# Kernel tuning notes

Hardware: AMD Instinct MI355X
Metric: run time of the kernel (lower is better)

The kernel has to match this reference:

```python
import jax, jax.numpy as jnp
import numpy as np

E, H = 512, 8
D = E // H  # head_dim = 64
NEG = jnp.finfo(jnp.float32).min


def setup_inputs() -> dict:
    key = jax.random.key(0)
    ks = jax.random.split(key, 12)
    s = 0.02
    return {
        "image": jax.random.normal(ks[0], (16, 197, E), jnp.float32),
        "text": jax.random.normal(ks[1], (64, 30, E), jnp.float32),
        "text_mask": jax.random.randint(ks[2], (64, 29), 0, 2).astype(bool),
        "Wq": jax.random.normal(ks[3], (D, D), jnp.float32) * s,
        "Wk": jax.random.normal(ks[4], (D, D), jnp.float32) * s,
        "Wv": jax.random.normal(ks[5], (D, D), jnp.float32) * s,
        "W_out": jax.random.normal(ks[6], (E, E), jnp.float32) * s,
        "b_out": jnp.zeros((E,), jnp.float32),
        "Wtv": jax.random.normal(ks[7], (D, D), jnp.float32) * s,
        "W_out_text": jax.random.normal(ks[8], (E, E), jnp.float32) * s,
        "b_out_text": jnp.zeros((E,), jnp.float32),
    }


def reference(image, text, text_mask, Wq, Wk, Wv, W_out, b_out, Wtv, W_out_text, b_out_text):
    I, Q, _ = image.shape
    T, K, _ = text.shape
    img = image.reshape(I, Q, H, D)
    txt = text.reshape(T, K, H, D)
    # per-head linear projections (torch Linear: y = x @ W.T)
    q = img @ Wq.T            # [I,Q,H,D]
    k = txt @ Wk.T            # [T,K,H,D]
    v = txt @ Wv.T            # [T,K,H,D]
    # cross-batch bidirectional attention energy [I,T,H,Q,K]
    energy = jnp.einsum('tkhd,iqhd->ithqk', k, q)
    # cls_present: pad mask with True at front along K
    mask = jnp.pad(text_mask, ((0, 0), (1, 0)), constant_values=True)  # [T,K]
    energy = jnp.where(mask[None, :, None, None, :], energy, NEG)
    scaled = energy / jnp.sqrt(jnp.float32(E))
    attention = jax.nn.softmax(scaled, axis=-1)       # over k (i2t)
    text_attention = jax.nn.softmax(scaled, axis=-2)  # over q (t2i)
    # i2t branch: [I,T,Q,H,D] -> [I,T,Q,E]
    out = jnp.einsum('ithqk,tkhd->itqhd', attention, v).reshape(I, T, Q, E)
    out = out @ W_out.T + b_out
    out = out.mean(axis=2)  # mean pool over image tokens -> [I,T,E]
    # t2i branch: [I,T,K,H,D] -> [I,T,K,E]
    tv = img @ Wtv.T  # [I,Q,H,D]
    out_text = jnp.einsum('ithqk,iqhd->itkhd', text_attention, tv).reshape(I, T, K, E)
    out_text = out_text @ W_out_text.T + b_out_text
    out_text = out_text.mean(axis=2)  # mean pool over text tokens -> [I,T,E]
    return (out, out_text, attention, text_attention)
```

## Files before the change

### kernel.cpp

```cpp
#include <hip/hip_runtime.h>
#include <hip/hip_bf16.h>
#include <cstdint>

#define I_ 16
#define T_ 64
#define Q_ 197
#define K_ 30
#define H_ 8
#define D_ 64
#define E_ 512

typedef float f32x2 __attribute__((ext_vector_type(2)));
typedef float f32x4 __attribute__((ext_vector_type(4)));
typedef short bf16x8 __attribute__((ext_vector_type(8)));

static constexpr float INV_SQRT_E = 0.044194173824159216f;
static constexpr float C197 = 1.0f / 197.0f;

#define OFF_QBF   0
#define OFF_KBF   806912
#define OFF_V     1298432
#define OFF_TV    2281472
#define OFF_ASUM  3895296
#define OFF_TASUM 4141056
#define OFF_POUT  5754880
#define OFF_PTXT  6279168

__global__ __launch_bounds__(512) void proj_kernel(
    const float* __restrict__ image, const float* __restrict__ text,
    const float* __restrict__ Wq, const float* __restrict__ Wk,
    const float* __restrict__ Wv, const float* __restrict__ Wtv,
    float* __restrict__ ws)
{
  const int NQ4 = (I_ * Q_) / 4;
  const int NT4 = (T_ * K_) / 4;
  int bb = blockIdx.x;
  const float* X; const float* W; int row0; int mode;
  if (bb < NQ4)             { X = image; W = Wq;  row0 = bb * 4;               mode = 0; }
  else if (bb < NQ4 + NT4)  { X = text;  W = Wk;  row0 = (bb - NQ4) * 4;       mode = 1; }
  else if (bb < NQ4 + 2*NT4){ X = text;  W = Wv;  row0 = (bb - NQ4 - NT4) * 4; mode = 2; }
  else                      { X = image; W = Wtv; row0 = (bb - NQ4 - 2*NT4)*4; mode = 3; }

  __shared__ float s_x[4][E_];
  __shared__ float s_w[D_][D_ + 1];
  int tid = threadIdx.x;
  for (int idx = tid; idx < D_ * D_; idx += 512) s_w[idx >> 6][idx & 63] = W[idx];
  #pragma unroll
  for (int rr = 0; rr < 4; ++rr) s_x[rr][tid] = X[(size_t)(row0 + rr) * E_ + tid];
  __syncthreads();

  int h = tid >> 6, dout = tid & 63;
  float a0 = 0.f, a1 = 0.f, a2 = 0.f, a3 = 0.f;
  #pragma unroll
  for (int d = 0; d < D_; ++d) {
    float w = s_w[dout][d];
    a0 = fmaf(s_x[0][h * 64 + d], w, a0);
    a1 = fmaf(s_x[1][h * 64 + d], w, a1);
    a2 = fmaf(s_x[2][h * 64 + d], w, a2);
    a3 = fmaf(s_x[3][h * 64 + d], w, a3);
  }
  if (mode <= 1) {
    __hip_bfloat16* Y = (__hip_bfloat16*)(ws + (mode == 0 ? OFF_QBF : OFF_KBF));
    Y[(size_t)(row0 + 0) * E_ + tid] = __float2bfloat16(a0);
    Y[(size_t)(row0 + 1) * E_ + tid] = __float2bfloat16(a1);
    Y[(size_t)(row0 + 2) * E_ + tid] = __float2bfloat16(a2);
    Y[(size_t)(row0 + 3) * E_ + tid] = __float2bfloat16(a3);
  } else {
    float* Y = ws + (mode == 2 ? OFF_V : OFF_TV);
    Y[(size_t)(row0 + 0) * E_ + tid] = a0;
    Y[(size_t)(row0 + 1) * E_ + tid] = a1;
    Y[(size_t)(row0 + 2) * E_ + tid] = a2;
    Y[(size_t)(row0 + 3) * E_ + tid] = a3;
  }
}

__global__ __launch_bounds__(256, 8) void attn_kernel(
    const __hip_bfloat16* __restrict__ qbf, const __hip_bfloat16* __restrict__ kbf,
    const int* __restrict__ text_mask,
    float* __restrict__ attn_out, float* __restrict__ tattn_out,
    float* __restrict__ A_sum, float* __restrict__ TA_sum)
{
  int b = blockIdx.x;
  int h = b & 7, t = (b >> 3) & 63, i = b >> 9;
  int tid = threadIdx.x;
  int w = tid >> 6, lane = tid & 63;
  int lr = lane & 15, lg = lane >> 4;

  __shared__ __hip_bfloat16 s_e[208 * 30];
  __shared__ float s_invrow[208];
  __shared__ float s_cd[4][32];
  __shared__ float s_ca[4][32];
  __shared__ float s_invd[32];
  __shared__ int   s_mask[32];

  if (tid < 32) s_mask[tid] = (tid == 0) ? 1 : (tid < K_ ? text_mask[t * (K_ - 1) + tid - 1] : 0);

  int m0 = (lr == 0) ? 1 : text_mask[t * (K_ - 1) + lr - 1];
  int m1 = (lr < 14) ? text_mask[t * (K_ - 1) + 15 + lr] : 0;

  const __hip_bfloat16* qb = qbf + ((size_t)(i * Q_) * H_ + h) * D_;
  const __hip_bfloat16* kb = kbf + ((size_t)(t * K_) * H_ + h) * D_;

  const bf16x8* bp0 = (const bf16x8*)(kb + (size_t)lr * (H_ * D_) + lg * 8);
  const bf16x8* bp1 = (const bf16x8*)(kb + (size_t)(16 + lr) * (H_ * D_) + lg * 8);
  bf16x8 b00 = bp0[0], b01 = bp0[4];
  bf16x8 b10 = bp1[0], b11 = bp1[4];

  float cd0 = 0.f, cd1 = 0.f, ca0 = 0.f, ca1 = 0.f;

  #pragma unroll
  for (int j = 0; j < 4; ++j) {
    int mt = w + 4 * j;
    if (mt < 13) {
      const bf16x8* ap = (const bf16x8*)(qb + (size_t)(mt * 16 + lr) * (H_ * D_) + lg * 8);
      bf16x8 a0 = ap[0], a1 = ap[4];
      f32x4 acc0 = {0.f, 0.f, 0.f, 0.f}, acc1 = {0.f, 0.f, 0.f, 0.f};
      acc0 = __builtin_amdgcn_mfma_f32_16x16x32_bf16(a0, b00, acc0, 0, 0, 0);
      acc0 = __builtin_amdgcn_mfma_f32_16x16x32_bf16(a1, b01, acc0, 0, 0, 0);
      acc1 = __builtin_amdgcn_mfma_f32_16x16x32_bf16(a0, b10, acc1, 0, 0, 0);
      acc1 = __builtin_amdgcn_mfma_f32_16x16x32_bf16(a1, b11, acc1, 0, 0, 0);
      int row0 = mt * 16 + lg * 4;
      float v0[4], v1[4];
      #pragma unroll
      for (int r = 0; r < 4; ++r) {
        bool vr = (row0 + r) < Q_;
        v0[r] = (vr && m0) ? __expf(acc0[r] * INV_SQRT_E) : 0.f;
        v1[r] = (vr && m1) ? __expf(acc1[r] * INV_SQRT_E) : 0.f;
        s_e[(row0 + r) * K_ + lr] = __float2bfloat16(v0[r]);
        if (lr < 14) s_e[(row0 + r) * K_ + 16 + lr] = __float2bfloat16(v1[r]);
      }
      #pragma unroll
      for (int r = 0; r < 4; ++r) {
        float s = v0[r] + v1[r];
        s += __shfl_xor(s, 1);
        s += __shfl_xor(s, 2);
        s += __shfl_xor(s, 4);
        s += __shfl_xor(s, 8);
        float iv = ((row0 + r) < Q_ && s > 0.f) ? (1.0f / s) : 0.f;
        if (lr == 0) s_invrow[row0 + r] = iv;
        cd0 += v0[r]; ca0 += v0[r] * iv;
        cd1 += v1[r]; ca1 += v1[r] * iv;
      }
    }
  }

  cd0 += __shfl_xor(cd0, 16); cd0 += __shfl_xor(cd0, 32);
  ca0 += __shfl_xor(ca0, 16); ca0 += __shfl_xor(ca0, 32);
  cd1 += __shfl_xor(cd1, 16); cd1 += __shfl_xor(cd1, 32);
  ca1 += __shfl_xor(ca1, 16); ca1 += __shfl_xor(ca1, 32);
  if (lane < 16) {
    s_cd[w][lr] = cd0; s_cd[w][lr + 16] = cd1;
    s_ca[w][lr] = ca0; s_ca[w][lr + 16] = ca1;
  }
  __syncthreads();

  if (tid < 32) {
    int col = tid;
    float d  = s_cd[0][col] + s_cd[1][col] + s_cd[2][col] + s_cd[3][col];
    float pa = s_ca[0][col] + s_ca[1][col] + s_ca[2][col] + s_ca[3][col];
    s_invd[col] = (s_mask[col] && d > 0.f) ? (1.0f / d) : 0.f;
    if (col < K_) A_sum[(size_t)b * K_ + col] = pa;
  }
  __syncthreads();

  if (tid < Q_) {
    float ta = 0.f;
    #pragma unroll
    for (int kk = 0; kk < K_; ++kk) {
      float ev = __bfloat162float(s_e[tid * K_ + kk]);
      ta += s_mask[kk] ? ev * s_invd[kk] : C197;
    }
    TA_sum[(size_t)b * Q_ + tid] = ta;
  }

  {
    int r0 = tid >> 4;
    int c2 = tid & 15;
    if (c2 < 15) {
      int mc0 = s_mask[2 * c2], mc1 = s_mask[2 * c2 + 1];
      float inv0 = s_invd[2 * c2], inv1 = s_invd[2 * c2 + 1];
      f32x2* adst = (f32x2*)(attn_out + (size_t)b * (Q_ * K_));
      f32x2* tdst = (f32x2*)(tattn_out + (size_t)b * (Q_ * K_));
      for (int row = r0; row < Q_; row += 16) {
        __hip_bfloat162 ev2 = *(const __hip_bfloat162*)&s_e[row * K_ + 2 * c2];
        float ex = __bfloat162float(ev2.x);
        float ey = __bfloat162float(ev2.y);
        float ir = s_invrow[row];
        f32x2 av  = { ex * ir, ey * ir };
        f32x2 tv2 = { mc0 ? ex * inv0 : C197, mc1 ? ey * inv1 : C197 };
        int o = row * 15 + c2;
        __builtin_nontemporal_store(av, &adst[o]);
        __builtin_nontemporal_store(tv2, &tdst[o]);
      }
    }
  }
}

__global__ __launch_bounds__(512) void pool_fused_kernel(
    const float* __restrict__ A_sum, const float* __restrict__ TA_sum,
    const float* __restrict__ ws_v, const float* __restrict__ ws_tv,
    float* __restrict__ P_out, float* __restrict__ P_txt)
{
  int bt = blockIdx.x;
  int t = bt & 63;
  int i = bt >> 6;
  int tid = threadIdx.x;
  int h = tid >> 6, d = tid & 63;
  __shared__ float s_A[H_ * K_];
  __shared__ float s_TA[H_ * Q_];
  if (tid < H_ * K_) s_A[tid] = A_sum[(size_t)bt * H_ * K_ + tid];
  for (int idx = tid; idx < H_ * Q_; idx += 512) s_TA[idx] = TA_sum[(size_t)bt * H_ * Q_ + idx];
  __syncthreads();

  {
    float a0 = 0.f, a1 = 0.f;
    #pragma unroll
    for (int kk = 0; kk < K_; kk += 2) {
      a0 = fmaf(s_A[h * K_ + kk],     ws_v[((size_t)(t * K_ + kk)     * H_ + h) * D_ + d], a0);
      a1 = fmaf(s_A[h * K_ + kk + 1], ws_v[((size_t)(t * K_ + kk + 1) * H_ + h) * D_ + d], a1);
    }
    P_out[(size_t)bt * E_ + tid] = (a0 + a1) * (1.0f / 197.0f);
  }

  {
    float a0 = 0.f, a1 = 0.f, a2 = 0.f, a3 = 0.f;
    int qq = 0;
    for (; qq + 4 <= Q_; qq += 4) {
      a0 = fmaf(s_TA[h * Q_ + qq + 0], ws_tv[((size_t)(i * Q_ + qq + 0) * H_ + h) * D_ + d], a0);
      a1 = fmaf(s_TA[h * Q_ + qq + 1], ws_tv[((size_t)(i * Q_ + qq + 1) * H_ + h) * D_ + d], a1);
      a2 = fmaf(s_TA[h * Q_ + qq + 2], ws_tv[((size_t)(i * Q_ + qq + 2) * H_ + h) * D_ + d], a2);
      a3 = fmaf(s_TA[h * Q_ + qq + 3], ws_tv[((size_t)(i * Q_ + qq + 3) * H_ + h) * D_ + d], a3);
    }
    for (; qq < Q_; ++qq)
      a0 = fmaf(s_TA[h * Q_ + qq], ws_tv[((size_t)(i * Q_ + qq) * H_ + h) * D_ + d], a0);
    P_txt[(size_t)bt * E_ + tid] = ((a0 + a1) + (a2 + a3)) * (1.0f / 30.0f);
  }
}

__global__ __launch_bounds__(256) void outproj_kernel(
    const float* __restrict__ Pout, const float* __restrict__ Ptxt,
    const float* __restrict__ W_out, const float* __restrict__ W_out_text,
    const float* __restrict__ b_out, const float* __restrict__ b_out_text,
    float* __restrict__ out_i2t, float* __restrict__ out_t2i)
{
  int z = blockIdx.z;
  const float* A    = z ? Ptxt : Pout;
  const float* W    = z ? W_out_text : W_out;
  const float* bias = z ? b_out_text : b_out;
  float* out        = z ? out_t2i : out_i2t;

  int r0 = blockIdx.x * 8;
  int eo = blockIdx.y * 256 + threadIdx.x;
  __shared__ float s_A[8][E_];
  for (int idx = threadIdx.x; idx < 8 * E_; idx += 256)
    s_A[idx >> 9][idx & 511] = A[(size_t)(r0 + (idx >> 9)) * E_ + (idx & 511)];
  __syncthreads();
  float acc[8] = {};
  const float4* wrow = (const float4*)(W + (size_t)eo * E_);
  for (int e4 = 0; e4 < E_ / 4; ++e4) {
    float4 w4 = wrow[e4];
    #pragma unroll
    for (int r = 0; r < 8; ++r) {
      acc[r] = fmaf(s_A[r][e4 * 4 + 0], w4.x, acc[r]);
      acc[r] = fmaf(s_A[r][e4 * 4 + 1], w4.y, acc[r]);
      acc[r] = fmaf(s_A[r][e4 * 4 + 2], w4.z, acc[r]);
      acc[r] = fmaf(s_A[r][e4 * 4 + 3], w4.w, acc[r]);
    }
  }
  float bv = bias[eo];
  #pragma unroll
  for (int r = 0; r < 8; ++r) out[(size_t)(r0 + r) * E_ + eo] = acc[r] + bv;
}

extern "C" void kernel_launch(void* const* d_in, const int* in_sizes, int n_in,
                              void* d_out, int out_size, void* d_ws, size_t ws_size,
                              hipStream_t stream)
{
  const float* image      = (const float*)d_in[0];
  const float* text       = (const float*)d_in[1];
  const int*   tmask      = (const int*)d_in[2];
  const float* Wq         = (const float*)d_in[3];
  const float* Wk         = (const float*)d_in[4];
  const float* Wv         = (const float*)d_in[5];
  const float* W_out      = (const float*)d_in[6];
  const float* b_out      = (const float*)d_in[7];
  const float* Wtv        = (const float*)d_in[8];
  const float* W_out_text = (const float*)d_in[9];
  const float* b_out_text = (const float*)d_in[10];

  float* out = (float*)d_out;
  float* ws  = (float*)d_ws;

  const __hip_bfloat16* qbf = (const __hip_bfloat16*)(ws + OFF_QBF);
  const __hip_bfloat16* kbf = (const __hip_bfloat16*)(ws + OFF_KBF);
  float* v     = ws + OFF_V;
  float* tv    = ws + OFF_TV;
  float* Asum  = ws + OFF_ASUM;
  float* TAsum = ws + OFF_TASUM;
  float* Pout  = ws + OFF_POUT;
  float* Ptxt  = ws + OFF_PTXT;

  float* out_i2t = out;
  float* out_t2i = out + (size_t)I_ * T_ * E_;
  float* attn    = out + (size_t)2 * I_ * T_ * E_;
  float* tattn   = attn + (size_t)I_ * T_ * H_ * Q_ * K_;

  proj_kernel<<<(I_*Q_)/4 + 2*((T_*K_)/4) + (I_*Q_)/4, 512, 0, stream>>>(image, text, Wq, Wk, Wv, Wtv, ws);
  attn_kernel<<<I_ * T_ * H_, 256, 0, stream>>>(qbf, kbf, tmask, attn, tattn, Asum, TAsum);
  pool_fused_kernel<<<I_ * T_, 512, 0, stream>>>(Asum, TAsum, v, tv, Pout, Ptxt);
  outproj_kernel<<<dim3(128, 2, 2), 256, 0, stream>>>(Pout, Ptxt, W_out, W_out_text,
                                                      b_out, b_out_text, out_i2t, out_t2i);
}
```

Baseline: 213.0 us.

## Use bf16 MFMA out-projection, regroup pooling for reuse, vectorize attention stores

```diff
diff --git a/kernel.cpp b/kernel.cpp
--- a/kernel.cpp
+++ b/kernel.cpp
@@ -16,6 +16,7 @@
 
 static constexpr float INV_SQRT_E = 0.044194173824159216f;
 static constexpr float C197 = 1.0f / 197.0f;
+static constexpr int   QK = Q_ * K_;
 
 #define OFF_QBF   0
 #define OFF_KBF   806912
@@ -23,18 +24,31 @@
 #define OFF_TV    2281472
 #define OFF_ASUM  3895296
 #define OFF_TASUM 4141056
-#define OFF_POUT  5754880
-#define OFF_PTXT  6279168
+#define OFF_PBF   5754880
+#define OFF_WBF   6279168
 
 __global__ __launch_bounds__(512) void proj_kernel(
     const float* __restrict__ image, const float* __restrict__ text,
     const float* __restrict__ Wq, const float* __restrict__ Wk,
     const float* __restrict__ Wv, const float* __restrict__ Wtv,
+    const float* __restrict__ W_out, const float* __restrict__ W_out_text,
     float* __restrict__ ws)
 {
   const int NQ4 = (I_ * Q_) / 4;
   const int NT4 = (T_ * K_) / 4;
   int bb = blockIdx.x;
+  int tid = threadIdx.x;
+
+  if (bb >= NQ4 + 2 * NT4 + NQ4) {
+    int row0 = (bb - (NQ4 + 2 * NT4 + NQ4)) * 4;
+    __hip_bfloat16* Wb = (__hip_bfloat16*)(ws + OFF_WBF);
+    const float* src = (row0 < 512) ? (W_out + row0 * E_) : (W_out_text + (row0 - 512) * E_);
+    #pragma unroll
+    for (int rr = 0; rr < 4; ++rr)
+      Wb[(size_t)(row0 + rr) * E_ + tid] = __float2bfloat16(src[rr * E_ + tid]);
+    return;
+  }
+
   const float* X; const float* W; int row0; int mode;
   if (bb < NQ4)             { X = image; W = Wq;  row0 = bb * 4;               mode = 0; }
   else if (bb < NQ4 + NT4)  { X = text;  W = Wk;  row0 = (bb - NQ4) * 4;       mode = 1; }
@@ -43,7 +57,6 @@
 
   __shared__ float s_x[4][E_];
   __shared__ float s_w[D_][D_ + 1];
-  int tid = threadIdx.x;
   for (int idx = tid; idx < D_ * D_; idx += 512) s_w[idx >> 6][idx & 63] = W[idx];
   #pragma unroll
   for (int rr = 0; rr < 4; ++rr) s_x[rr][tid] = X[(size_t)(row0 + rr) * E_ + tid];
@@ -174,102 +187,149 @@
   }
 
   {
-    int r0 = tid >> 4;
-    int c2 = tid & 15;
-    if (c2 < 15) {
-      int mc0 = s_mask[2 * c2], mc1 = s_mask[2 * c2 + 1];
-      float inv0 = s_invd[2 * c2], inv1 = s_invd[2 * c2 + 1];
-      f32x2* adst = (f32x2*)(attn_out + (size_t)b * (Q_ * K_));
-      f32x2* tdst = (f32x2*)(tattn_out + (size_t)b * (Q_ * K_));
-      for (int row = r0; row < Q_; row += 16) {
-        __hip_bfloat162 ev2 = *(const __hip_bfloat162*)&s_e[row * K_ + 2 * c2];
-        float ex = __bfloat162float(ev2.x);
-        float ey = __bfloat162float(ev2.y);
-        float ir = s_invrow[row];
-        f32x2 av  = { ex * ir, ey * ir };
-        f32x2 tv2 = { mc0 ? ex * inv0 : C197, mc1 ? ey * inv1 : C197 };
-        int o = row * 15 + c2;
-        __builtin_nontemporal_store(av, &adst[o]);
-        __builtin_nontemporal_store(tv2, &tdst[o]);
+    float* abase = attn_out  + (size_t)b * QK;
+    float* tbase = tattn_out + (size_t)b * QK;
+    int head = (b & 1) ? 2 : 0;
+    if (tid == 0) {
+      int e0 = head ? 0 : (QK - 2);
+      float ex = __bfloat162float(s_e[e0]);
+      float ey = __bfloat162float(s_e[e0 + 1]);
+      int r0 = e0 / K_, c0 = e0 - r0 * K_;
+      int r1 = (e0 + 1) / K_, c1 = (e0 + 1) - r1 * K_;
+      f32x2 av = { ex * s_invrow[r0], ey * s_invrow[r1] };
+      f32x2 tv2 = { s_mask[c0] ? ex * s_invd[c0] : C197,
+                    s_mask[c1] ? ey * s_invd[c1] : C197 };
+      __builtin_nontemporal_store(av,  (f32x2*)(abase + e0));
+      __builtin_nontemporal_store(tv2, (f32x2*)(tbase + e0));
+    }
+    for (int fi = tid; fi < 1477; fi += 256) {
+      int base = head + fi * 4;
+      float ev[4]; int rw[4]; int cl[4];
+      #pragma unroll
+      for (int e = 0; e < 4; ++e) {
+        int idx = base + e;
+        ev[e] = __bfloat162float(s_e[idx]);
+        rw[e] = idx / K_;
+        cl[e] = idx - rw[e] * K_;
       }
-    }
-  }
-}
-
-__global__ __launch_bounds__(512) void pool_fused_kernel(
-    const float* __restrict__ A_sum, const float* __restrict__ TA_sum,
-    const float* __restrict__ ws_v, const float* __restrict__ ws_tv,
-    float* __restrict__ P_out, float* __restrict__ P_txt)
-{
-  int bt = blockIdx.x;
-  int t = bt & 63;
-  int i = bt >> 6;
-  int tid = threadIdx.x;
-  int h = tid >> 6, d = tid & 63;
-  __shared__ float s_A[H_ * K_];
-  __shared__ float s_TA[H_ * Q_];
-  if (tid < H_ * K_) s_A[tid] = A_sum[(size_t)bt * H_ * K_ + tid];
-  for (int idx = tid; idx < H_ * Q_; idx += 512) s_TA[idx] = TA_sum[(size_t)bt * H_ * Q_ + idx];
+      f32x4 av, tv4;
+      #pragma unroll
+      for (int e = 0; e < 4; ++e) {
+        av[e]  = ev[e] * s_invrow[rw[e]];
+        tv4[e] = s_mask[cl[e]] ? ev[e] * s_invd[cl[e]] : C197;
+      }
+      __builtin_nontemporal_store(av,  (f32x4*)(abase + base));
+      __builtin_nontemporal_store(tv4, (f32x4*)(tbase + base));
+    }
+  }
+}
+
+__global__ __launch_bounds__(512) void pool_i2t_kernel(
+    const float* __restrict__ A_sum, const float* __restrict__ ws_v,
+    __hip_bfloat16* __restrict__ Pbf)
+{
+  int bb = blockIdx.x;
+  int h = bb & 7, t = bb >> 3;
+  int tid = threadIdx.x;
+  __shared__ float s_A[I_ * K_];
+  __shared__ float s_v[K_ * D_];
+  for (int idx = tid; idx < I_ * K_; idx += 512) {
+    int ii = idx / K_, kk = idx - ii * K_;
+    s_A[idx] = A_sum[((size_t)((ii * T_ + t) * H_ + h)) * K_ + kk];
+  }
+  for (int idx = tid; idx < K_ * D_; idx += 512) {
+    int kk = idx >> 6, d = idx & 63;
+    s_v[idx] = ws_v[((size_t)(t * K_ + kk) * H_ + h) * D_ + d];
+  }
   __syncthreads();
-
-  {
-    float a0 = 0.f, a1 = 0.f;
+  int ii = tid >> 5, dp = tid & 31, d0 = dp * 2;
+  float a0 = 0.f, a1 = 0.f;
+  #pragma unroll
+  for (int kk = 0; kk < K_; ++kk) {
+    float av = s_A[ii * K_ + kk];
+    a0 = fmaf(av, s_v[kk * 64 + d0], a0);
+    a1 = fmaf(av, s_v[kk * 64 + d0 + 1], a1);
+  }
+  __hip_bfloat162 pv;
+  pv.x = __float2bfloat16(a0 * C197);
+  pv.y = __float2bfloat16(a1 * C197);
+  *(__hip_bfloat162*)&Pbf[(size_t)(ii * T_ + t) * E_ + h * 64 + d0] = pv;
+}
+
+__global__ __launch_bounds__(512) void pool_t2i_kernel(
+    const float* __restrict__ TA_sum, const float* __restrict__ ws_tv,
+    __hip_bfloat16* __restrict__ Pbf)
+{
+  int bb = blockIdx.x;
+  int h = bb & 7, i = bb >> 3;
+  int tid = threadIdx.x;
+  __shared__ float s_TA[T_ * Q_];
+  __shared__ float s_tv[32 * D_];
+  for (int idx = tid; idx < T_ * Q_; idx += 512) {
+    int tt = idx / Q_, qq = idx - tt * Q_;
+    s_TA[idx] = TA_sum[((size_t)((i * T_ + tt) * H_ + h)) * Q_ + qq];
+  }
+  int t = tid >> 3, dg = tid & 7, d0 = dg * 8;
+  float acc[8] = {};
+  for (int c = 0; c < 7; ++c) {
+    int q0 = c * 32;
+    int n = (q0 + 32 <= Q_) ? 32 : (Q_ - q0);
+    __syncthreads();
+    for (int idx = tid; idx < n * D_; idx += 512) {
+      int qq = idx >> 6, d = idx & 63;
+      s_tv[idx] = ws_tv[((size_t)((i * Q_ + q0 + qq) * H_ + h)) * D_ + d];
+    }
+    __syncthreads();
+    for (int qq = 0; qq < n; ++qq) {
+      float ta = s_TA[t * Q_ + q0 + qq];
+      #pragma unroll
+      for (int dd = 0; dd < 8; ++dd)
+        acc[dd] = fmaf(ta, s_tv[qq * 64 + d0 + dd], acc[dd]);
+    }
+  }
+  __hip_bfloat16* dst = &Pbf[(size_t)(1024 + i * T_ + t) * E_ + h * 64 + d0];
+  #pragma unroll
+  for (int p = 0; p < 4; ++p) {
+    __hip_bfloat162 pv;
+    pv.x = __float2bfloat16(acc[2 * p] * (1.0f / 30.0f));
+    pv.y = __float2bfloat16(acc[2 * p + 1] * (1.0f / 30.0f));
+    *(__hip_bfloat162*)&dst[2 * p] = pv;
+  }
+}
+
+__global__ __launch_bounds__(256) void outproj_mfma_kernel(
+    const __hip_bfloat16* __restrict__ Pbf, const __hip_bfloat16* __restrict__ Wbf,
+    const float* __restrict__ b_out, const float* __restrict__ b_out_text,
+    float* __restrict__ out)
+{
+  int mt = blockIdx.x;
+  int z = (mt >= 64);
+  int tid = threadIdx.x;
+  int w = tid >> 6, lane = tid & 63;
+  int lr = lane & 15, lg = lane >> 4;
+
+  const __hip_bfloat16* A = Pbf + (size_t)(mt * 16 + lr) * E_ + lg * 8;
+  const __hip_bfloat16* B = Wbf + (size_t)(z * 512) * E_;
+  f32x4 acc[8] = {};
+  for (int ks = 0; ks < 16; ++ks) {
+    bf16x8 a = *(const bf16x8*)(A + ks * 32);
     #pragma unroll
-    for (int kk = 0; kk < K_; kk += 2) {
-      a0 = fmaf(s_A[h * K_ + kk],     ws_v[((size_t)(t * K_ + kk)     * H_ + h) * D_ + d], a0);
-      a1 = fmaf(s_A[h * K_ + kk + 1], ws_v[((size_t)(t * K_ + kk + 1) * H_ + h) * D_ + d], a1);
-    }
-    P_out[(size_t)bt * E_ + tid] = (a0 + a1) * (1.0f / 197.0f);
-  }
-
-  {
-    float a0 = 0.f, a1 = 0.f, a2 = 0.f, a3 = 0.f;
-    int qq = 0;
-    for (; qq + 4 <= Q_; qq += 4) {
-      a0 = fmaf(s_TA[h * Q_ + qq + 0], ws_tv[((size_t)(i * Q_ + qq + 0) * H_ + h) * D_ + d], a0);
-      a1 = fmaf(s_TA[h * Q_ + qq + 1], ws_tv[((size_t)(i * Q_ + qq + 1) * H_ + h) * D_ + d], a1);
-      a2 = fmaf(s_TA[h * Q_ + qq + 2], ws_tv[((size_t)(i * Q_ + qq + 2) * H_ + h) * D_ + d], a2);
-      a3 = fmaf(s_TA[h * Q_ + qq + 3], ws_tv[((size_t)(i * Q_ + qq + 3) * H_ + h) * D_ + d], a3);
-    }
-    for (; qq < Q_; ++qq)
-      a0 = fmaf(s_TA[h * Q_ + qq], ws_tv[((size_t)(i * Q_ + qq) * H_ + h) * D_ + d], a0);
-    P_txt[(size_t)bt * E_ + tid] = ((a0 + a1) + (a2 + a3)) * (1.0f / 30.0f);
-  }
-}
-
-__global__ __launch_bounds__(256) void outproj_kernel(
-    const float* __restrict__ Pout, const float* __restrict__ Ptxt,
-    const float* __restrict__ W_out, const float* __restrict__ W_out_text,
-    const float* __restrict__ b_out, const float* __restrict__ b_out_text,
-    float* __restrict__ out_i2t, float* __restrict__ out_t2i)
-{
-  int z = blockIdx.z;
-  const float* A    = z ? Ptxt : Pout;
-  const float* W    = z ? W_out_text : W_out;
+    for (int nt = 0; nt < 8; ++nt) {
+      int n0 = w * 128 + nt * 16;
+      bf16x8 bv = *(const bf16x8*)(B + (size_t)(n0 + lr) * E_ + ks * 32 + lg * 8);
+      acc[nt] = __builtin_amdgcn_mfma_f32_16x16x32_bf16(a, bv, acc[nt], 0, 0, 0);
+    }
+  }
   const float* bias = z ? b_out_text : b_out;
-  float* out        = z ? out_t2i : out_i2t;
-
-  int r0 = blockIdx.x * 8;
-  int eo = blockIdx.y * 256 + threadIdx.x;
-  __shared__ float s_A[8][E_];
-  for (int idx = threadIdx.x; idx < 8 * E_; idx += 256)
-    s_A[idx >> 9][idx & 511] = A[(size_t)(r0 + (idx >> 9)) * E_ + (idx & 511)];
-  __syncthreads();
-  float acc[8] = {};
-  const float4* wrow = (const float4*)(W + (size_t)eo * E_);
-  for (int e4 = 0; e4 < E_ / 4; ++e4) {
-    float4 w4 = wrow[e4];
+  int row0 = mt * 16 + lg * 4;
+  #pragma unroll
+  for (int nt = 0; nt < 8; ++nt) {
+    int n = w * 128 + nt * 16 + lr;
+    float bv = bias[n];
     #pragma unroll
-    for (int r = 0; r < 8; ++r) {
-      acc[r] = fmaf(s_A[r][e4 * 4 + 0], w4.x, acc[r]);
-      acc[r] = fmaf(s_A[r][e4 * 4 + 1], w4.y, acc[r]);
-      acc[r] = fmaf(s_A[r][e4 * 4 + 2], w4.z, acc[r]);
-      acc[r] = fmaf(s_A[r][e4 * 4 + 3], w4.w, acc[r]);
-    }
-  }
-  float bv = bias[eo];
-  #pragma unroll
-  for (int r = 0; r < 8; ++r) out[(size_t)(r0 + r) * E_ + eo] = acc[r] + bv;
+    for (int r = 0; r < 4; ++r)
+      out[(size_t)(row0 + r) * E_ + n] = acc[nt][r] + bv;
+  }
 }
 
 extern "C" void kernel_launch(void* const* d_in, const int* in_sizes, int n_in,
@@ -297,17 +357,17 @@
   float* tv    = ws + OFF_TV;
   float* Asum  = ws + OFF_ASUM;
   float* TAsum = ws + OFF_TASUM;
-  float* Pout  = ws + OFF_POUT;
-  float* Ptxt  = ws + OFF_PTXT;
-
-  float* out_i2t = out;
-  float* out_t2i = out + (size_t)I_ * T_ * E_;
+  __hip_bfloat16* Pbf = (__hip_bfloat16*)(ws + OFF_PBF);
+  __hip_bfloat16* Wbf = (__hip_bfloat16*)(ws + OFF_WBF);
+
   float* attn    = out + (size_t)2 * I_ * T_ * E_;
   float* tattn   = attn + (size_t)I_ * T_ * H_ * Q_ * K_;
 
-  proj_kernel<<<(I_*Q_)/4 + 2*((T_*K_)/4) + (I_*Q_)/4, 512, 0, stream>>>(image, text, Wq, Wk, Wv, Wtv, ws);
+  const int NQ4 = (I_ * Q_) / 4, NT4 = (T_ * K_) / 4;
+  proj_kernel<<<NQ4 + 2 * NT4 + NQ4 + 256, 512, 0, stream>>>(
+      image, text, Wq, Wk, Wv, Wtv, W_out, W_out_text, ws);
   attn_kernel<<<I_ * T_ * H_, 256, 0, stream>>>(qbf, kbf, tmask, attn, tattn, Asum, TAsum);
-  pool_fused_kernel<<<I_ * T_, 512, 0, stream>>>(Asum, TAsum, v, tv, Pout, Ptxt);
-  outproj_kernel<<<dim3(128, 2, 2), 256, 0, stream>>>(Pout, Ptxt, W_out, W_out_text,
-                                                      b_out, b_out_text, out_i2t, out_t2i);
-}
+  pool_i2t_kernel<<<T_ * H_, 512, 0, stream>>>(Asum, v, Pbf);
+  pool_t2i_kernel<<<I_ * H_, 512, 0, stream>>>(TAsum, tv, Pbf);
+  outproj_mfma_kernel<<<128, 256, 0, stream>>>(Pbf, Wbf, b_out, b_out_text, out);
+}
```

New measurement: 516.6 us. 2.43x slower.
